# Optimization experiments

Measured on AMD Instinct MI355X. Metric: run time of the kernel, lower is better.

Reference implementation:

```python
import jax, jax.numpy as jnp
from jax import lax
import numpy as np

IN, HID, NCLS, B, S = 360, 64, 5, 64, 128
MH_CONST = 2.0 / (np.sqrt(3.0) * np.pi ** 0.25)


def setup_inputs() -> dict:
    key = jax.random.key(0)
    ks = jax.random.split(key, 24)
    g = lambda i, shape, s=0.05: jax.random.normal(ks[i], shape, jnp.float32) * s
    inp = {
        'x_seq': jax.random.normal(ks[0], (B, S, IN), jnp.float32),
        # WavKANLinear params (out=64, in=360)
        'wav_scale': jnp.ones((HID, IN), jnp.float32),
        'wav_translation': jnp.zeros((HID, IN), jnp.float32),
        'wav_weights': g(1, (HID, IN)),
        'base_weight': g(2, (HID, IN)),
        # BatchNorm1d (eval mode, running stats)
        'bn_gamma': jnp.ones((HID,), jnp.float32),
        'bn_beta': jnp.zeros((HID,), jnp.float32),
        'bn_mean': jnp.zeros((HID,), jnp.float32),
        'bn_var': jnp.ones((HID,), jnp.float32),
        # LayerNorm(64)
        'ln_gamma': jnp.ones((HID,), jnp.float32),
        'ln_beta': jnp.zeros((HID,), jnp.float32),
        # bidirectional GRU, 1 layer, hidden=64
        'gru_w_ih_f': g(3, (3 * HID, HID)), 'gru_w_hh_f': g(4, (3 * HID, HID)),
        'gru_b_ih_f': g(5, (3 * HID,)), 'gru_b_hh_f': g(6, (3 * HID,)),
        'gru_w_ih_b': g(7, (3 * HID, HID)), 'gru_w_hh_b': g(8, (3 * HID, HID)),
        'gru_b_ih_b': g(9, (3 * HID,)), 'gru_b_hh_b': g(10, (3 * HID,)),
        # classifier: Linear(128,64) -> ReLU -> Linear(64,5)
        'fc1_w': g(11, (HID, 2 * HID)), 'fc1_b': jnp.zeros((HID,), jnp.float32),
        'fc2_w': g(12, (NCLS, HID)), 'fc2_b': jnp.zeros((NCLS,), jnp.float32),
    }
    return inp


def _gru_dir(x_sbf, w_ih, w_hh, b_ih, b_hh, reverse):
    # x_sbf: (S, B, F). Returns final hidden (B, H). PyTorch GRU equations.
    Bn = x_sbf.shape[1]
    H = w_hh.shape[1]
    gi_all = jnp.einsum('sbf,gf->sbg', x_sbf, w_ih) + b_ih  # precompute input gates

    def step(h, gi):
        gh = h @ w_hh.T + b_hh
        i_r, i_z, i_n = jnp.split(gi, 3, axis=-1)
        h_r, h_z, h_n = jnp.split(gh, 3, axis=-1)
        r = jax.nn.sigmoid(i_r + h_r)
        z = jax.nn.sigmoid(i_z + h_z)
        n = jnp.tanh(i_n + r * h_n)
        h_new = (1.0 - z) * n + z * h
        return h_new, None

    h0 = jnp.zeros((Bn, H), x_sbf.dtype)
    h_final, _ = lax.scan(step, h0, gi_all, reverse=reverse)
    return h_final


def reference(x_seq, wav_scale, wav_translation, wav_weights, base_weight,
              bn_gamma, bn_beta, bn_mean, bn_var, ln_gamma, ln_beta,
              gru_w_ih_f, gru_w_hh_f, gru_b_ih_f, gru_b_hh_f,
              gru_w_ih_b, gru_w_hh_b, gru_b_ih_b, gru_b_hh_b,
              fc1_w, fc1_b, fc2_w, fc2_b):
    b, s, f = x_seq.shape
    x_flat = x_seq.reshape(b * s, f)  # (N, 360)

    # --- WavKANLinear (mexican_hat) ---
    x_scaled = (x_flat[:, None, :] - wav_translation[None]) / wav_scale[None]  # (N, 64, 360)
    wavelet = MH_CONST * (x_scaled * x_scaled - 1.0) * jnp.exp(-0.5 * x_scaled * x_scaled)
    wav_out = jnp.einsum('noi,oi->no', wavelet, wav_weights)  # (N, 64)
    base_out = jax.nn.silu(x_flat) @ base_weight.T
    combined = wav_out + base_out
    # BatchNorm1d eval mode
    x_emb = (combined - bn_mean) * lax.rsqrt(bn_var + 1e-5) * bn_gamma + bn_beta

    # --- LayerNorm(64) ---
    mu = jnp.mean(x_emb, axis=-1, keepdims=True)
    var = jnp.mean(jnp.square(x_emb - mu), axis=-1, keepdims=True)
    x_emb = (x_emb - mu) * lax.rsqrt(var + 1e-5) * ln_gamma + ln_beta
    # dropout is identity in eval mode

    x_sbf = x_emb.reshape(b, s, HID).swapaxes(0, 1)  # (S, B, 64)

    # --- bidirectional GRU, take final hiddens ---
    h_fwd = _gru_dir(x_sbf, gru_w_ih_f, gru_w_hh_f, gru_b_ih_f, gru_b_hh_f, False)
    h_bwd = _gru_dir(x_sbf, gru_w_ih_b, gru_w_hh_b, gru_b_ih_b, gru_b_hh_b, True)
    hidden_cat = jnp.concatenate([h_fwd, h_bwd], axis=1)  # (B, 128)

    # --- classifier ---
    h = jax.nn.relu(hidden_cat @ fc1_w.T + fc1_b)
    logits = h @ fc2_w.T + fc2_b
    return logits
```

## Files before the change

kernel.cpp:

```cpp
#include <hip/hip_runtime.h>

#define IN_F   360
#define HIDN   64
#define NCLS   5
#define BATCH  64
#define SEQ    128
#define NROWS  (BATCH*SEQ)

#define WS_FLAG  0
#define WS_WPACK 16
#define WS_WFAST 92176
#define WS_WT4   138256
#define WS_XEMB  162832
#define WS_GI    687120
#define WS_HC    3832848

#define LOG2E        1.4426950408889634f
#define NEG_HALF_L2E (-0.7213475204444817f)

__device__ __forceinline__ float fast_rcp(float x) { return __builtin_amdgcn_rcpf(x); }
__device__ __forceinline__ float fast_rsq(float x) { return __builtin_amdgcn_rsqf(x); }
__device__ __forceinline__ float sigmoid_(float x) {
    x = fminf(fmaxf(x, -60.0f), 60.0f);
    return fast_rcp(1.0f + exp2f(-LOG2E * x));
}
__device__ __forceinline__ float tanh_(float x) {
    x = fminf(fmaxf(x, -30.0f), 30.0f);
    float e = exp2f(-2.8853900817779268f * x);
    return (1.0f - e) * fast_rcp(1.0f + e);
}
__device__ __forceinline__ float readlane_f(float v, int l) {
    return __int_as_float(__builtin_amdgcn_readlane(__float_as_int(v), l));
}

__global__ __launch_bounds__(256) void prep_kernel(
    const float* __restrict__ scale, const float* __restrict__ trans,
    const float* __restrict__ ww,    const float* __restrict__ bw,
    const float* __restrict__ wihf,  const float* __restrict__ wihb,
    float* __restrict__ ws) {
    int idx = blockIdx.x * 256 + threadIdx.x;
    float4* wpack  = (float4*)(ws + WS_WPACK);
    float2* wfast2 = (float2*)(ws + WS_WFAST);
    float*  wT4    = ws + WS_WT4;
    int*    flagp  = (int*)(ws + WS_FLAG);
    if (idx < 64 * IN_F) {
        int o = idx & 63, i = idx >> 6;
        float s  = scale[o * IN_F + i];
        float tr = trans[o * IN_F + i];
        if (s != 1.0f || tr != 0.0f) atomicOr(flagp, 1);
        float a  = 1.0f / s;
        float b  = -tr * a;
        float wq = 0.8673250705840776f * ww[o * IN_F + i];
        float bb = bw[o * IN_F + i];
        wpack[i * 64 + o] = make_float4(a, b, wq, bb);
        wfast2[(i >> 1) * 128 + o * 2 + (i & 1)] = make_float2(wq, bb);
    }
    int idx2 = idx - 64 * IN_F;
    if (idx2 >= 0 && idx2 < 24576) {
        int e = idx2 & 3; int rest = idx2 >> 2;
        int g = rest % 384; int k4 = rest / 384;
        int k = k4 * 4 + e; int dir = g / 192; int gg = g - dir * 192;
        const float* src = dir ? wihb : wihf;
        wT4[idx2] = src[gg * 64 + k];
    }
}

__global__ __launch_bounds__(256) void wavkan_kernel(
    const float* __restrict__ x_seq,
    const float* __restrict__ bn_g, const float* __restrict__ bn_b,
    const float* __restrict__ bn_m, const float* __restrict__ bn_v,
    const float* __restrict__ ln_g, const float* __restrict__ ln_b,
    const float* __restrict__ ws_c, float* __restrict__ x_emb) {
    __shared__ float2 xs_lds[16 * IN_F];
    int t = threadIdx.x;
    int row0 = blockIdx.x * 16;
    int o = t & 63, grp = t >> 6;
    int fast = (*(const int*)(ws_c + WS_FLAG)) == 0;

    float acc0 = 0.f, acc1 = 0.f, acc2 = 0.f, acc3 = 0.f;

    if (fast) {
        for (int idx = t; idx < 16 * IN_F; idx += 256) {
            int r = idx / IN_F, i = idx - r * IN_F;
            float x = x_seq[(row0 + r) * IN_F + i];
            float u = x * x;
            float phi = (u - 1.0f) * exp2f(u * NEG_HALF_L2E);
            float sl  = x * fast_rcp(1.0f + exp2f(-LOG2E * x));
            xs_lds[idx] = make_float2(phi, sl);
        }
        __syncthreads();
        const float4* wf4 = (const float4*)(ws_c + WS_WFAST);
        const float4* xs4 = (const float4*)xs_lds;
        const float4* xr0 = xs4 + (grp * 4 + 0) * 180;
        const float4* xr1 = xs4 + (grp * 4 + 1) * 180;
        const float4* xr2 = xs4 + (grp * 4 + 2) * 180;
        const float4* xr3 = xs4 + (grp * 4 + 3) * 180;
        #pragma unroll 2
        for (int i2 = 0; i2 < 180; ++i2) {
            float4 wp = wf4[i2 * 64 + o];
            float4 a = xr0[i2];
            acc0 = fmaf(a.x, wp.x, acc0); acc0 = fmaf(a.y, wp.y, acc0);
            acc0 = fmaf(a.z, wp.z, acc0); acc0 = fmaf(a.w, wp.w, acc0);
            float4 b = xr1[i2];
            acc1 = fmaf(b.x, wp.x, acc1); acc1 = fmaf(b.y, wp.y, acc1);
            acc1 = fmaf(b.z, wp.z, acc1); acc1 = fmaf(b.w, wp.w, acc1);
            float4 c = xr2[i2];
            acc2 = fmaf(c.x, wp.x, acc2); acc2 = fmaf(c.y, wp.y, acc2);
            acc2 = fmaf(c.z, wp.z, acc2); acc2 = fmaf(c.w, wp.w, acc2);
            float4 d = xr3[i2];
            acc3 = fmaf(d.x, wp.x, acc3); acc3 = fmaf(d.y, wp.y, acc3);
            acc3 = fmaf(d.z, wp.z, acc3); acc3 = fmaf(d.w, wp.w, acc3);
        }
    } else {
        for (int idx = t; idx < 16 * IN_F; idx += 256) {
            int r = idx / IN_F, i = idx - r * IN_F;
            float x = x_seq[(row0 + r) * IN_F + i];
            float sl = x * fast_rcp(1.0f + exp2f(-LOG2E * x));
            xs_lds[idx] = make_float2(x, sl);
        }
        __syncthreads();
        const float4* wpack = (const float4*)(ws_c + WS_WPACK);
        const float2* xr0 = xs_lds + (grp * 4 + 0) * IN_F;
        const float2* xr1 = xs_lds + (grp * 4 + 1) * IN_F;
        const float2* xr2 = xs_lds + (grp * 4 + 2) * IN_F;
        const float2* xr3 = xs_lds + (grp * 4 + 3) * IN_F;
        for (int i = 0; i < IN_F; ++i) {
            float4 wp = wpack[i * 64 + o];
            {
                float2 xs = xr0[i];
                float xsc = fmaf(xs.x, wp.x, wp.y); float u = xsc * xsc;
                float e = exp2f(u * NEG_HALF_L2E);
                acc0 = fmaf((u - 1.0f) * e, wp.z, acc0);
                acc0 = fmaf(xs.y, wp.w, acc0);
            }
            {
                float2 xs = xr1[i];
                float xsc = fmaf(xs.x, wp.x, wp.y); float u = xsc * xsc;
                float e = exp2f(u * NEG_HALF_L2E);
                acc1 = fmaf((u - 1.0f) * e, wp.z, acc1);
                acc1 = fmaf(xs.y, wp.w, acc1);
            }
            {
                float2 xs = xr2[i];
                float xsc = fmaf(xs.x, wp.x, wp.y); float u = xsc * xsc;
                float e = exp2f(u * NEG_HALF_L2E);
                acc2 = fmaf((u - 1.0f) * e, wp.z, acc2);
                acc2 = fmaf(xs.y, wp.w, acc2);
            }
            {
                float2 xs = xr3[i];
                float xsc = fmaf(xs.x, wp.x, wp.y); float u = xsc * xsc;
                float e = exp2f(u * NEG_HALF_L2E);
                acc3 = fmaf((u - 1.0f) * e, wp.z, acc3);
                acc3 = fmaf(xs.y, wp.w, acc3);
            }
        }
    }

    float bscale = bn_g[o] * fast_rsq(bn_v[o] + 1e-5f);
    float bshift = fmaf(-bn_m[o], bscale, bn_b[o]);
    float lg = ln_g[o], lb = ln_b[o];
    float vals[4] = {acc0, acc1, acc2, acc3};
    #pragma unroll
    for (int rr = 0; rr < 4; ++rr) {
        float y = fmaf(vals[rr], bscale, bshift);
        float s = y;
        #pragma unroll
        for (int m = 1; m < 64; m <<= 1) s += __shfl_xor(s, m, 64);
        float mu = s * (1.0f / 64.0f);
        float d = y - mu;
        float s2 = d * d;
        #pragma unroll
        for (int m = 1; m < 64; m <<= 1) s2 += __shfl_xor(s2, m, 64);
        float rstd = fast_rsq(s2 * (1.0f / 64.0f) + 1e-5f);
        x_emb[(row0 + grp * 4 + rr) * 64 + o] = fmaf(d * rstd, lg, lb);
    }
}

__global__ __launch_bounds__(384) void gi_kernel(
    const float* __restrict__ ws_c,
    const float* __restrict__ bihf, const float* __restrict__ bihb,
    float* __restrict__ gi) {
    __shared__ __align__(16) float xs[32 * 64];
    const float4* wT4   = (const float4*)(ws_c + WS_WT4);
    const float*  x_emb = ws_c + WS_XEMB;
    int t = threadIdx.x;
    int row0 = blockIdx.x * 32;
    {
        const float4* src = (const float4*)(x_emb + row0 * 64);
        float4* dst = (float4*)xs;
        for (int i = t; i < 512; i += 384) dst[i] = src[i];
    }
    int dir = t / 192, gg = t - dir * 192;
    float bih = dir ? bihb[gg] : bihf[gg];
    float4 w[16];
    #pragma unroll
    for (int k4 = 0; k4 < 16; ++k4) w[k4] = wT4[k4 * 384 + t];
    __syncthreads();
    for (int r = 0; r < 32; r += 2) {
        const float4* x0 = (const float4*)(xs + r * 64);
        const float4* x1 = (const float4*)(xs + r * 64 + 64);
        float a0 = bih, a1 = 0.f, b0 = bih, b1 = 0.f;
        #pragma unroll
        for (int k4 = 0; k4 < 16; k4 += 2) {
            float4 xv = x0[k4];     float4 wv = w[k4];
            a0 = fmaf(xv.x, wv.x, a0); a0 = fmaf(xv.y, wv.y, a0);
            a0 = fmaf(xv.z, wv.z, a0); a0 = fmaf(xv.w, wv.w, a0);
            float4 xu = x0[k4 + 1]; float4 wu = w[k4 + 1];
            a1 = fmaf(xu.x, wu.x, a1); a1 = fmaf(xu.y, wu.y, a1);
            a1 = fmaf(xu.z, wu.z, a1); a1 = fmaf(xu.w, wu.w, a1);
            float4 yv = x1[k4];
            b0 = fmaf(yv.x, wv.x, b0); b0 = fmaf(yv.y, wv.y, b0);
            b0 = fmaf(yv.z, wv.z, b0); b0 = fmaf(yv.w, wv.w, b0);
            float4 yu = x1[k4 + 1];
            b1 = fmaf(yu.x, wu.x, b1); b1 = fmaf(yu.y, wu.y, b1);
            b1 = fmaf(yu.z, wu.z, b1); b1 = fmaf(yu.w, wu.w, b1);
        }
        gi[(row0 + r) * 384 + t]     = a0 + a1;
        gi[(row0 + r + 1) * 384 + t] = b0 + b1;
    }
}

__global__ __launch_bounds__(192, 1) void gru_kernel(
    const float* __restrict__ ws_c,
    const float* __restrict__ whhf, const float* __restrict__ bhhf,
    const float* __restrict__ whhb, const float* __restrict__ bhhb,
    float* __restrict__ hc) {
    __shared__ __align__(16) float gi_l[64 * 192];
    __shared__ __align__(16) float ex[2][192];
    const float* gi = ws_c + WS_GI;
    int t = threadIdx.x, lane = t & 63, g = t >> 6;
    int b = blockIdx.x & 63, dir = blockIdx.x >> 6;
    const float* whh = dir ? whhb : whhf;
    const float* bhh = dir ? bhhb : bhhf;

    float w[64];
    {
        const float4* wrow = (const float4*)(whh + t * 64);
        #pragma unroll
        for (int q = 0; q < 16; ++q) {
            float4 a = wrow[q];
            w[4*q] = a.x; w[4*q+1] = a.y; w[4*q+2] = a.z; w[4*q+3] = a.w;
        }
    }
    float bias = bhh[t];

    const float* gsrc = gi + (size_t)(b * SEQ) * 384 + dir * 192 + t;
#define GOFF(s) ((dir ? (SEQ - 1 - (s)) : (s)) * 384)
    #pragma unroll 8
    for (int q = 0; q < 64; ++q) gi_l[q * 192 + t] = gsrc[GOFF(q)];
    float h = 0.0f;
    __syncthreads();

    for (int ss = 0; ss < SEQ; ++ss) {
        if (ss == 64) {
            __syncthreads();
            #pragma unroll 8
            for (int q = 0; q < 64; ++q) gi_l[q * 192 + t] = gsrc[GOFF(64 + q)];
            __syncthreads();
        }
        int ssl = ss & 63, p = ss & 1;
        float acc0 = bias, acc1 = 0.f;
        #pragma unroll
        for (int c = 0; c < 4; ++c) {
            float sh[16];
            #pragma unroll
            for (int j = 0; j < 16; ++j) sh[j] = readlane_f(h, c * 16 + j);
            #pragma unroll
            for (int j = 0; j < 16; j += 2) {
                acc0 = fmaf(w[c * 16 + j],     sh[j],     acc0);
                acc1 = fmaf(w[c * 16 + j + 1], sh[j + 1], acc1);
            }
        }
        float a = acc0 + acc1;
        float giv = gi_l[ssl * 192 + t];
        float v = (g == 2) ? a : sigmoid_(giv + a);
        ex[p][t] = v;
        __syncthreads();
        float r   = ex[p][lane];
        float z   = ex[p][64 + lane];
        float an  = ex[p][128 + lane];
        float i_n = gi_l[ssl * 192 + 128 + lane];
        float n = tanh_(fmaf(r, an, i_n));
        h = fmaf(z, h - n, n);
    }
#undef GOFF
    if (g == 0) hc[b * 128 + dir * 64 + lane] = h;
}

__global__ __launch_bounds__(64) void head_kernel(
    const float* __restrict__ ws_c,
    const float* __restrict__ fc1w, const float* __restrict__ fc1b,
    const float* __restrict__ fc2w, const float* __restrict__ fc2b,
    float* __restrict__ out) {
    __shared__ __align__(16) float hr[128];
    __shared__ float h1[64];
    const float* hc = ws_c + WS_HC;
    int bb = blockIdx.x, t = threadIdx.x;
    hr[t]      = hc[bb * 128 + t];
    hr[64 + t] = hc[bb * 128 + 64 + t];
    __syncthreads();
    float acc = fc1b[t];
    const float4* w4 = (const float4*)(fc1w + t * 128);
    const float4* h4 = (const float4*)hr;
    #pragma unroll 8
    for (int k4 = 0; k4 < 32; ++k4) {
        float4 wv = w4[k4]; float4 hv = h4[k4];
        acc = fmaf(hv.x, wv.x, acc); acc = fmaf(hv.y, wv.y, acc);
        acc = fmaf(hv.z, wv.z, acc); acc = fmaf(hv.w, wv.w, acc);
    }
    h1[t] = fmaxf(acc, 0.0f);
    __syncthreads();
    if (t < NCLS) {
        float acc2 = fc2b[t];
        const float* wr = fc2w + t * 64;
        #pragma unroll 8
        for (int k = 0; k < 64; ++k) acc2 = fmaf(h1[k], wr[k], acc2);
        out[bb * NCLS + t] = acc2;
    }
}

extern "C" void kernel_launch(void* const* d_in, const int* in_sizes, int n_in,
                              void* d_out, int out_size, void* d_ws, size_t ws_size,
                              hipStream_t stream) {
    const float* x_seq = (const float*)d_in[0];
    const float* wscal = (const float*)d_in[1];
    const float* wtran = (const float*)d_in[2];
    const float* wwght = (const float*)d_in[3];
    const float* bwght = (const float*)d_in[4];
    const float* bn_g  = (const float*)d_in[5];
    const float* bn_b  = (const float*)d_in[6];
    const float* bn_m  = (const float*)d_in[7];
    const float* bn_v  = (const float*)d_in[8];
    const float* ln_g  = (const float*)d_in[9];
    const float* ln_b  = (const float*)d_in[10];
    const float* wihf  = (const float*)d_in[11];
    const float* whhf  = (const float*)d_in[12];
    const float* bihf  = (const float*)d_in[13];
    const float* bhhf  = (const float*)d_in[14];
    const float* wihb  = (const float*)d_in[15];
    const float* whhb  = (const float*)d_in[16];
    const float* bihb  = (const float*)d_in[17];
    const float* bhhb  = (const float*)d_in[18];
    const float* fc1w  = (const float*)d_in[19];
    const float* fc1b  = (const float*)d_in[20];
    const float* fc2w  = (const float*)d_in[21];
    const float* fc2b  = (const float*)d_in[22];
    float* ws  = (float*)d_ws;
    float* out = (float*)d_out;

    hipMemsetAsync(ws + WS_FLAG, 0, sizeof(int), stream);
    hipLaunchKernelGGL(prep_kernel, dim3(186), dim3(256), 0, stream,
                       wscal, wtran, wwght, bwght, wihf, wihb, ws);
    hipLaunchKernelGGL(wavkan_kernel, dim3(NROWS / 16), dim3(256), 0, stream,
                       x_seq, bn_g, bn_b, bn_m, bn_v, ln_g, ln_b, ws, ws + WS_XEMB);
    hipLaunchKernelGGL(gi_kernel, dim3(NROWS / 32), dim3(384), 0, stream,
                       ws, bihf, bihb, ws + WS_GI);
    hipLaunchKernelGGL(gru_kernel, dim3(128), dim3(192), 0, stream,
                       ws, whhf, bhhf, whhb, bhhb, ws + WS_HC);
    hipLaunchKernelGGL(head_kernel, dim3(64), dim3(64), 0, stream,
                       ws, fc1w, fc1b, fc2w, fc2b, out);
}
```

Baseline: 233.3 us.

## Merge forward and backward GRU directions into one block per batch

The GRU kernel now runs both directions for a batch element in a single 384-thread block (64 blocks instead of 128 blocks of 192). The gate-input staging in shared memory shrinks from 64-step to 32-step chunks, refilled every 32 steps. This halves the block count on a GPU with many CUs, and each per-step barrier now synchronizes 6 waves instead of 3, with more frequent refill stalls. The likely aim is lower shared memory per block or better SIMD packing, but the serial recurrence stays the same length.

```diff
diff --git a/kernel.cpp b/kernel.cpp
--- a/kernel.cpp
+++ b/kernel.cpp
@@ -221,71 +221,73 @@
     }
 }
 
-__global__ __launch_bounds__(192, 1) void gru_kernel(
+__global__ __launch_bounds__(384, 1) void gru_kernel(
     const float* __restrict__ ws_c,
     const float* __restrict__ whhf, const float* __restrict__ bhhf,
     const float* __restrict__ whhb, const float* __restrict__ bhhb,
     float* __restrict__ hc) {
-    __shared__ __align__(16) float gi_l[64 * 192];
-    __shared__ __align__(16) float ex[2][192];
+    __shared__ __align__(16) float gi_l[2][32][192];
+    __shared__ __align__(16) float ex[2][2][192];
     const float* gi = ws_c + WS_GI;
-    int t = threadIdx.x, lane = t & 63, g = t >> 6;
-    int b = blockIdx.x & 63, dir = blockIdx.x >> 6;
-    const float* whh = dir ? whhb : whhf;
-    const float* bhh = dir ? bhhb : bhhf;
+    int t = threadIdx.x, lane = t & 63, wv = t >> 6;
+    int g = wv >> 1, c = wv & 1;
+    int b = blockIdx.x;
+    const float* whh = c ? whhb : whhf;
+    const float* bhh = c ? bhhb : bhhf;
 
     float w[64];
     {
-        const float4* wrow = (const float4*)(whh + t * 64);
+        const float4* wrow = (const float4*)(whh + (g * 64 + lane) * 64);
         #pragma unroll
         for (int q = 0; q < 16; ++q) {
             float4 a = wrow[q];
             w[4*q] = a.x; w[4*q+1] = a.y; w[4*q+2] = a.z; w[4*q+3] = a.w;
         }
     }
-    float bias = bhh[t];
-
-    const float* gsrc = gi + (size_t)(b * SEQ) * 384 + dir * 192 + t;
-#define GOFF(s) ((dir ? (SEQ - 1 - (s)) : (s)) * 384)
+    float bias = bhh[g * 64 + lane];
+
+    int cc = t / 192, ct = t - cc * 192;
+    const float* gsrc = gi + (size_t)(b * SEQ) * 384 + cc * 192 + ct;
+#define GOFF_C(ch, s) ((int)((ch) ? (SEQ - 1 - (s)) : (s)) * 384)
     #pragma unroll 8
-    for (int q = 0; q < 64; ++q) gi_l[q * 192 + t] = gsrc[GOFF(q)];
+    for (int q = 0; q < 32; ++q) gi_l[cc][q][ct] = gsrc[GOFF_C(cc, q)];
     float h = 0.0f;
     __syncthreads();
 
     for (int ss = 0; ss < SEQ; ++ss) {
-        if (ss == 64) {
-            __syncthreads();
-            #pragma unroll 8
-            for (int q = 0; q < 64; ++q) gi_l[q * 192 + t] = gsrc[GOFF(64 + q)];
-            __syncthreads();
-        }
-        int ssl = ss & 63, p = ss & 1;
+        int ssl = ss & 31, p = ss & 1;
+        float giv = gi_l[c][ssl][g * 64 + lane];
+        float inv = gi_l[c][ssl][128 + lane];
         float acc0 = bias, acc1 = 0.f;
         #pragma unroll
-        for (int c = 0; c < 4; ++c) {
+        for (int c4 = 0; c4 < 4; ++c4) {
             float sh[16];
             #pragma unroll
-            for (int j = 0; j < 16; ++j) sh[j] = readlane_f(h, c * 16 + j);
+            for (int j = 0; j < 16; ++j) sh[j] = readlane_f(h, c4 * 16 + j);
             #pragma unroll
             for (int j = 0; j < 16; j += 2) {
-                acc0 = fmaf(w[c * 16 + j],     sh[j],     acc0);
-                acc1 = fmaf(w[c * 16 + j + 1], sh[j + 1], acc1);
+                acc0 = fmaf(w[c4 * 16 + j],     sh[j],     acc0);
+                acc1 = fmaf(w[c4 * 16 + j + 1], sh[j + 1], acc1);
             }
         }
         float a = acc0 + acc1;
-        float giv = gi_l[ssl * 192 + t];
         float v = (g == 2) ? a : sigmoid_(giv + a);
-        ex[p][t] = v;
+        ex[p][c][g * 64 + lane] = v;
         __syncthreads();
-        float r   = ex[p][lane];
-        float z   = ex[p][64 + lane];
-        float an  = ex[p][128 + lane];
-        float i_n = gi_l[ssl * 192 + 128 + lane];
-        float n = tanh_(fmaf(r, an, i_n));
+        float r  = ex[p][c][lane];
+        float z  = ex[p][c][64 + lane];
+        float an = ex[p][c][128 + lane];
+        float n = tanh_(fmaf(r, an, inv));
         h = fmaf(z, h - n, n);
-    }
-#undef GOFF
-    if (g == 0) hc[b * 128 + dir * 64 + lane] = h;
+        if ((ss & 31) == 31 && ss != SEQ - 1) {
+            int base = ss + 1;
+            #pragma unroll 8
+            for (int q = 0; q < 32; ++q) gi_l[cc][q][ct] = gsrc[GOFF_C(cc, base + q)];
+            __syncthreads();
+        }
+    }
+#undef GOFF_C
+    if (g == 0) hc[b * 128 + c * 64 + lane] = h;
 }
 
 __global__ __launch_bounds__(64) void head_kernel(
@@ -356,7 +358,7 @@
                        x_seq, bn_g, bn_b, bn_m, bn_v, ln_g, ln_b, ws, ws + WS_XEMB);
     hipLaunchKernelGGL(gi_kernel, dim3(NROWS / 32), dim3(384), 0, stream,
                        ws, bihf, bihb, ws + WS_GI);
-    hipLaunchKernelGGL(gru_kernel, dim3(128), dim3(192), 0, stream,
+    hipLaunchKernelGGL(gru_kernel, dim3(64), dim3(384), 0, stream,
                        ws, whhf, bhhf, whhb, bhhb, ws + WS_HC);
     hipLaunchKernelGGL(head_kernel, dim3(64), dim3(64), 0, stream,
                        ws, fc1w, fc1b, fc2w, fc2b, out);
```

Measured after the change: 262.5 us. 12.5% more time.

## Fuse WavKAN embedding and GRU input-gate projection into one kernel

Applied to the files above, without the earlier changes.

Merges the WavKAN+BatchNorm+LayerNorm kernel and the GRU input-gate GEMM into a single 512-thread kernel. Each block handles 32 rows in two 16-row stages and keeps the normalized embeddings in LDS instead of writing them to global memory and reading them back. This removes one launch and the x_emb round trip, at the cost of a larger block with more LDS, fewer blocks overall, and 128 threads idle during the gate phase. Separately, the GRU loop now loads its input-gate values from LDS before the recurrent dot product, so that load latency is hidden.

```diff
diff --git a/kernel.cpp b/kernel.cpp
--- a/kernel.cpp
+++ b/kernel.cpp
@@ -65,159 +65,128 @@
     }
 }
 
-__global__ __launch_bounds__(256) void wavkan_kernel(
+__global__ __launch_bounds__(512) void wavgi_kernel(
     const float* __restrict__ x_seq,
     const float* __restrict__ bn_g, const float* __restrict__ bn_b,
     const float* __restrict__ bn_m, const float* __restrict__ bn_v,
     const float* __restrict__ ln_g, const float* __restrict__ ln_b,
-    const float* __restrict__ ws_c, float* __restrict__ x_emb) {
+    const float* __restrict__ ws_c,
+    const float* __restrict__ bihf, const float* __restrict__ bihb,
+    float* __restrict__ gi) {
     __shared__ float2 xs_lds[16 * IN_F];
+    __shared__ __align__(16) float xs2[32 * 64];
     int t = threadIdx.x;
-    int row0 = blockIdx.x * 16;
+    int row0 = blockIdx.x * 32;
     int o = t & 63, grp = t >> 6;
     int fast = (*(const int*)(ws_c + WS_FLAG)) == 0;
-
-    float acc0 = 0.f, acc1 = 0.f, acc2 = 0.f, acc3 = 0.f;
-
-    if (fast) {
-        for (int idx = t; idx < 16 * IN_F; idx += 256) {
-            int r = idx / IN_F, i = idx - r * IN_F;
-            float x = x_seq[(row0 + r) * IN_F + i];
-            float u = x * x;
-            float phi = (u - 1.0f) * exp2f(u * NEG_HALF_L2E);
-            float sl  = x * fast_rcp(1.0f + exp2f(-LOG2E * x));
-            xs_lds[idx] = make_float2(phi, sl);
-        }
-        __syncthreads();
-        const float4* wf4 = (const float4*)(ws_c + WS_WFAST);
-        const float4* xs4 = (const float4*)xs_lds;
-        const float4* xr0 = xs4 + (grp * 4 + 0) * 180;
-        const float4* xr1 = xs4 + (grp * 4 + 1) * 180;
-        const float4* xr2 = xs4 + (grp * 4 + 2) * 180;
-        const float4* xr3 = xs4 + (grp * 4 + 3) * 180;
-        #pragma unroll 2
-        for (int i2 = 0; i2 < 180; ++i2) {
-            float4 wp = wf4[i2 * 64 + o];
-            float4 a = xr0[i2];
-            acc0 = fmaf(a.x, wp.x, acc0); acc0 = fmaf(a.y, wp.y, acc0);
-            acc0 = fmaf(a.z, wp.z, acc0); acc0 = fmaf(a.w, wp.w, acc0);
-            float4 b = xr1[i2];
-            acc1 = fmaf(b.x, wp.x, acc1); acc1 = fmaf(b.y, wp.y, acc1);
-            acc1 = fmaf(b.z, wp.z, acc1); acc1 = fmaf(b.w, wp.w, acc1);
-            float4 c = xr2[i2];
-            acc2 = fmaf(c.x, wp.x, acc2); acc2 = fmaf(c.y, wp.y, acc2);
-            acc2 = fmaf(c.z, wp.z, acc2); acc2 = fmaf(c.w, wp.w, acc2);
-            float4 d = xr3[i2];
-            acc3 = fmaf(d.x, wp.x, acc3); acc3 = fmaf(d.y, wp.y, acc3);
-            acc3 = fmaf(d.z, wp.z, acc3); acc3 = fmaf(d.w, wp.w, acc3);
-        }
-    } else {
-        for (int idx = t; idx < 16 * IN_F; idx += 256) {
-            int r = idx / IN_F, i = idx - r * IN_F;
-            float x = x_seq[(row0 + r) * IN_F + i];
-            float sl = x * fast_rcp(1.0f + exp2f(-LOG2E * x));
-            xs_lds[idx] = make_float2(x, sl);
-        }
-        __syncthreads();
-        const float4* wpack = (const float4*)(ws_c + WS_WPACK);
-        const float2* xr0 = xs_lds + (grp * 4 + 0) * IN_F;
-        const float2* xr1 = xs_lds + (grp * 4 + 1) * IN_F;
-        const float2* xr2 = xs_lds + (grp * 4 + 2) * IN_F;
-        const float2* xr3 = xs_lds + (grp * 4 + 3) * IN_F;
-        for (int i = 0; i < IN_F; ++i) {
-            float4 wp = wpack[i * 64 + o];
-            {
-                float2 xs = xr0[i];
-                float xsc = fmaf(xs.x, wp.x, wp.y); float u = xsc * xsc;
-                float e = exp2f(u * NEG_HALF_L2E);
-                acc0 = fmaf((u - 1.0f) * e, wp.z, acc0);
-                acc0 = fmaf(xs.y, wp.w, acc0);
-            }
-            {
-                float2 xs = xr1[i];
-                float xsc = fmaf(xs.x, wp.x, wp.y); float u = xsc * xsc;
-                float e = exp2f(u * NEG_HALF_L2E);
-                acc1 = fmaf((u - 1.0f) * e, wp.z, acc1);
-                acc1 = fmaf(xs.y, wp.w, acc1);
-            }
-            {
-                float2 xs = xr2[i];
-                float xsc = fmaf(xs.x, wp.x, wp.y); float u = xsc * xsc;
-                float e = exp2f(u * NEG_HALF_L2E);
-                acc2 = fmaf((u - 1.0f) * e, wp.z, acc2);
-                acc2 = fmaf(xs.y, wp.w, acc2);
-            }
-            {
-                float2 xs = xr3[i];
-                float xsc = fmaf(xs.x, wp.x, wp.y); float u = xsc * xsc;
-                float e = exp2f(u * NEG_HALF_L2E);
-                acc3 = fmaf((u - 1.0f) * e, wp.z, acc3);
-                acc3 = fmaf(xs.y, wp.w, acc3);
-            }
-        }
-    }
 
     float bscale = bn_g[o] * fast_rsq(bn_v[o] + 1e-5f);
     float bshift = fmaf(-bn_m[o], bscale, bn_b[o]);
     float lg = ln_g[o], lb = ln_b[o];
-    float vals[4] = {acc0, acc1, acc2, acc3};
-    #pragma unroll
-    for (int rr = 0; rr < 4; ++rr) {
-        float y = fmaf(vals[rr], bscale, bshift);
-        float s = y;
+
+    for (int st = 0; st < 2; ++st) {
+        if (st) __syncthreads();
+        float acc0 = 0.f, acc1 = 0.f;
+        if (fast) {
+            for (int idx = t; idx < 16 * IN_F; idx += 512) {
+                int r = idx / IN_F, i = idx - r * IN_F;
+                float x = x_seq[(row0 + st * 16 + r) * IN_F + i];
+                float u = x * x;
+                float phi = (u - 1.0f) * exp2f(u * NEG_HALF_L2E);
+                float sl  = x * fast_rcp(1.0f + exp2f(-LOG2E * x));
+                xs_lds[idx] = make_float2(phi, sl);
+            }
+            __syncthreads();
+            const float4* wf4 = (const float4*)(ws_c + WS_WFAST);
+            const float4* xs4 = (const float4*)xs_lds;
+            const float4* xr0 = xs4 + (grp * 2 + 0) * 180;
+            const float4* xr1 = xs4 + (grp * 2 + 1) * 180;
+            #pragma unroll 2
+            for (int i2 = 0; i2 < 180; ++i2) {
+                float4 wp = wf4[i2 * 64 + o];
+                float4 a = xr0[i2];
+                acc0 = fmaf(a.x, wp.x, acc0); acc0 = fmaf(a.y, wp.y, acc0);
+                acc0 = fmaf(a.z, wp.z, acc0); acc0 = fmaf(a.w, wp.w, acc0);
+                float4 b = xr1[i2];
+                acc1 = fmaf(b.x, wp.x, acc1); acc1 = fmaf(b.y, wp.y, acc1);
+                acc1 = fmaf(b.z, wp.z, acc1); acc1 = fmaf(b.w, wp.w, acc1);
+            }
+        } else {
+            for (int idx = t; idx < 16 * IN_F; idx += 512) {
+                int r = idx / IN_F, i = idx - r * IN_F;
+                float x = x_seq[(row0 + st * 16 + r) * IN_F + i];
+                float sl = x * fast_rcp(1.0f + exp2f(-LOG2E * x));
+                xs_lds[idx] = make_float2(x, sl);
+            }
+            __syncthreads();
+            const float4* wpack = (const float4*)(ws_c + WS_WPACK);
+            const float2* xr0 = xs_lds + (grp * 2 + 0) * IN_F;
+            const float2* xr1 = xs_lds + (grp * 2 + 1) * IN_F;
+            for (int i = 0; i < IN_F; ++i) {
+                float4 wp = wpack[i * 64 + o];
+                {
+                    float2 xs = xr0[i];
+                    float xsc = fmaf(xs.x, wp.x, wp.y); float u = xsc * xsc;
+                    float e = exp2f(u * NEG_HALF_L2E);
+                    acc0 = fmaf((u - 1.0f) * e, wp.z, acc0);
+                    acc0 = fmaf(xs.y, wp.w, acc0);
+                }
+                {
+                    float2 xs = xr1[i];
+                    float xsc = fmaf(xs.x, wp.x, wp.y); float u = xsc * xsc;
+                    float e = exp2f(u * NEG_HALF_L2E);
+                    acc1 = fmaf((u - 1.0f) * e, wp.z, acc1);
+                    acc1 = fmaf(xs.y, wp.w, acc1);
+                }
+            }
+        }
+        float vals[2] = {acc0, acc1};
         #pragma unroll
-        for (int m = 1; m < 64; m <<= 1) s += __shfl_xor(s, m, 64);
-        float mu = s * (1.0f / 64.0f);
-        float d = y - mu;
-        float s2 = d * d;
+        for (int rr = 0; rr < 2; ++rr) {
+            float y = fmaf(vals[rr], bscale, bshift);
+            float s = y;
+            #pragma unroll
+            for (int m = 1; m < 64; m <<= 1) s += __shfl_xor(s, m, 64);
+            float mu = s * (1.0f / 64.0f);
+            float d = y - mu;
+            float s2 = d * d;
+            #pragma unroll
+            for (int m = 1; m < 64; m <<= 1) s2 += __shfl_xor(s2, m, 64);
+            float rstd = fast_rsq(s2 * (1.0f / 64.0f) + 1e-5f);
+            xs2[(st * 16 + grp * 2 + rr) * 64 + o] = fmaf(d * rstd, lg, lb);
+        }
+    }
+    __syncthreads();
+
+    if (t < 384) {
+        const float4* wT4 = (const float4*)(ws_c + WS_WT4);
+        int dir = t / 192, gg = t - dir * 192;
+        float bih = dir ? bihb[gg] : bihf[gg];
+        float4 w[16];
         #pragma unroll
-        for (int m = 1; m < 64; m <<= 1) s2 += __shfl_xor(s2, m, 64);
-        float rstd = fast_rsq(s2 * (1.0f / 64.0f) + 1e-5f);
-        x_emb[(row0 + grp * 4 + rr) * 64 + o] = fmaf(d * rstd, lg, lb);
-    }
-}
-
-__global__ __launch_bounds__(384) void gi_kernel(
-    const float* __restrict__ ws_c,
-    const float* __restrict__ bihf, const float* __restrict__ bihb,
-    float* __restrict__ gi) {
-    __shared__ __align__(16) float xs[32 * 64];
-    const float4* wT4   = (const float4*)(ws_c + WS_WT4);
-    const float*  x_emb = ws_c + WS_XEMB;
-    int t = threadIdx.x;
-    int row0 = blockIdx.x * 32;
-    {
-        const float4* src = (const float4*)(x_emb + row0 * 64);
-        float4* dst = (float4*)xs;
-        for (int i = t; i < 512; i += 384) dst[i] = src[i];
-    }
-    int dir = t / 192, gg = t - dir * 192;
-    float bih = dir ? bihb[gg] : bihf[gg];
-    float4 w[16];
-    #pragma unroll
-    for (int k4 = 0; k4 < 16; ++k4) w[k4] = wT4[k4 * 384 + t];
-    __syncthreads();
-    for (int r = 0; r < 32; r += 2) {
-        const float4* x0 = (const float4*)(xs + r * 64);
-        const float4* x1 = (const float4*)(xs + r * 64 + 64);
-        float a0 = bih, a1 = 0.f, b0 = bih, b1 = 0.f;
-        #pragma unroll
-        for (int k4 = 0; k4 < 16; k4 += 2) {
-            float4 xv = x0[k4];     float4 wv = w[k4];
-            a0 = fmaf(xv.x, wv.x, a0); a0 = fmaf(xv.y, wv.y, a0);
-            a0 = fmaf(xv.z, wv.z, a0); a0 = fmaf(xv.w, wv.w, a0);
-            float4 xu = x0[k4 + 1]; float4 wu = w[k4 + 1];
-            a1 = fmaf(xu.x, wu.x, a1); a1 = fmaf(xu.y, wu.y, a1);
-            a1 = fmaf(xu.z, wu.z, a1); a1 = fmaf(xu.w, wu.w, a1);
-            float4 yv = x1[k4];
-            b0 = fmaf(yv.x, wv.x, b0); b0 = fmaf(yv.y, wv.y, b0);
-            b0 = fmaf(yv.z, wv.z, b0); b0 = fmaf(yv.w, wv.w, b0);
-            float4 yu = x1[k4 + 1];
-            b1 = fmaf(yu.x, wu.x, b1); b1 = fmaf(yu.y, wu.y, b1);
-            b1 = fmaf(yu.z, wu.z, b1); b1 = fmaf(yu.w, wu.w, b1);
-        }
-        gi[(row0 + r) * 384 + t]     = a0 + a1;
-        gi[(row0 + r + 1) * 384 + t] = b0 + b1;
+        for (int k4 = 0; k4 < 16; ++k4) w[k4] = wT4[k4 * 384 + t];
+        for (int r = 0; r < 32; r += 2) {
+            const float4* x0 = (const float4*)(xs2 + r * 64);
+            const float4* x1 = (const float4*)(xs2 + r * 64 + 64);
+            float a0 = bih, a1 = 0.f, b0 = bih, b1 = 0.f;
+            #pragma unroll
+            for (int k4 = 0; k4 < 16; k4 += 2) {
+                float4 xv = x0[k4];     float4 wv = w[k4];
+                a0 = fmaf(xv.x, wv.x, a0); a0 = fmaf(xv.y, wv.y, a0);
+                a0 = fmaf(xv.z, wv.z, a0); a0 = fmaf(xv.w, wv.w, a0);
+                float4 xu = x0[k4 + 1]; float4 wu = w[k4 + 1];
+                a1 = fmaf(xu.x, wu.x, a1); a1 = fmaf(xu.y, wu.y, a1);
+                a1 = fmaf(xu.z, wu.z, a1); a1 = fmaf(xu.w, wu.w, a1);
+                float4 yv = x1[k4];
+                b0 = fmaf(yv.x, wv.x, b0); b0 = fmaf(yv.y, wv.y, b0);
+                b0 = fmaf(yv.z, wv.z, b0); b0 = fmaf(yv.w, wv.w, b0);
+                float4 yu = x1[k4 + 1];
+                b1 = fmaf(yu.x, wu.x, b1); b1 = fmaf(yu.y, wu.y, b1);
+                b1 = fmaf(yu.z, wu.z, b1); b1 = fmaf(yu.w, wu.w, b1);
+            }
+            gi[(row0 + r) * 384 + t]     = a0 + a1;
+            gi[(row0 + r + 1) * 384 + t] = b0 + b1;
+        }
     }
 }
 
@@ -260,6 +229,8 @@
             __syncthreads();
         }
         int ssl = ss & 63, p = ss & 1;
+        float giv = gi_l[ssl * 192 + t];
+        float inv = gi_l[ssl * 192 + 128 + lane];
         float acc0 = bias, acc1 = 0.f;
         #pragma unroll
         for (int c = 0; c < 4; ++c) {
@@ -273,15 +244,13 @@
             }
         }
         float a = acc0 + acc1;
-        float giv = gi_l[ssl * 192 + t];
         float v = (g == 2) ? a : sigmoid_(giv + a);
         ex[p][t] = v;
         __syncthreads();
         float r   = ex[p][lane];
         float z   = ex[p][64 + lane];
         float an  = ex[p][128 + lane];
-        float i_n = gi_l[ssl * 192 + 128 + lane];
-        float n = tanh_(fmaf(r, an, i_n));
+        float n = tanh_(fmaf(r, an, inv));
         h = fmaf(z, h - n, n);
     }
 #undef GOFF
@@ -352,10 +321,9 @@
     hipMemsetAsync(ws + WS_FLAG, 0, sizeof(int), stream);
     hipLaunchKernelGGL(prep_kernel, dim3(186), dim3(256), 0, stream,
                        wscal, wtran, wwght, bwght, wihf, wihb, ws);
-    hipLaunchKernelGGL(wavkan_kernel, dim3(NROWS / 16), dim3(256), 0, stream,
-                       x_seq, bn_g, bn_b, bn_m, bn_v, ln_g, ln_b, ws, ws + WS_XEMB);
-    hipLaunchKernelGGL(gi_kernel, dim3(NROWS / 32), dim3(384), 0, stream,
-                       ws, bihf, bihb, ws + WS_GI);
+    hipLaunchKernelGGL(wavgi_kernel, dim3(NROWS / 32), dim3(512), 0, stream,
+                       x_seq, bn_g, bn_b, bn_m, bn_v, ln_g, ln_b, ws,
+                       bihf, bihb, ws + WS_GI);
     hipLaunchKernelGGL(gru_kernel, dim3(128), dim3(192), 0, stream,
                        ws, whhf, bhhf, whhb, bhhb, ws + WS_HC);
     hipLaunchKernelGGL(head_kernel, dim3(64), dim3(64), 0, stream,
```

Result: slower. 240.8 us (+3.2%).
